# Kernel tuning notes

Hardware: AMD Instinct MI355X
Metric: run time of the kernel (lower is better)

Reference implementation:

```python
import jax, jax.numpy as jnp
import numpy as np

N = 16        # n_var
L = 16        # max_lags
H = 16        # hidden_dim
B = 32768     # batch
G = N * N     # n_var^2 groups


def setup_inputs() -> dict:
    key = jax.random.key(0)
    ks = jax.random.split(key, 8)
    x = jax.random.normal(ks[0], (B, G, L), dtype=jnp.float32)
    causal = jax.random.randint(ks[1], (N, N, L), 0, 2, dtype=jnp.int32)
    # torch Conv1d init: U(-sqrt(k), sqrt(k)), k = 1/(in_channels_per_group*kernel)
    s1 = 1.0 / np.sqrt(L)        # conv1: in/group=1, kernel=L
    s2 = 1.0 / np.sqrt(H)        # conv2: in/group=H, kernel=1
    s3 = 1.0 / np.sqrt(N * H)    # conv3: in/group=N*H, kernel=1
    W1 = jax.random.uniform(ks[2], (G, H, L), jnp.float32, -s1, s1)
    b1 = jax.random.uniform(ks[3], (G, H), jnp.float32, -s1, s1)
    W2 = jax.random.uniform(ks[4], (G, H, H), jnp.float32, -s2, s2)
    b2 = jax.random.uniform(ks[5], (G, H), jnp.float32, -s2, s2)
    W3 = jax.random.uniform(ks[6], (N, N * H), jnp.float32, -s3, s3)
    b3 = jax.random.uniform(ks[7], (N,), jnp.float32, -s3, s3)
    return {"x": x, "causal": causal, "W1": W1, "b1": b1,
            "W2": W2, "b2": b2, "W3": W3, "b3": b3}


def reference(x, causal, W1, b1, W2, b2, W3, b3):
    # mask = ~causal_matrix.bool() -> masked_fill with 0 == multiply by causal!=0
    mask = (causal != 0).reshape(1, G, L).astype(x.dtype)
    xm = x * mask                                          # [B, G, L]
    # conv1: per-group (1 -> H) over the full lag window (output length 1)
    h1 = jax.nn.sigmoid(jnp.einsum('bgl,ghl->bgh', xm, W1) + b1)   # [B, G, H]
    # conv2: per-group (H -> H) 1x1; W2[g, out, in]
    h2 = jax.nn.sigmoid(jnp.einsum('bgh,gkh->bgk', h1, W2) + b2)   # [B, G, H]
    # conv3: groups = n_var, per variable (N*H -> 1) 1x1
    h2f = h2.reshape(-1, N, N * H)                          # [B, N, N*H]
    out = jnp.einsum('bvm,vm->bv', h2f, W3) + b3            # [B, N]
    return out
```

## Files before the change

kernel.cpp:

```cpp
#include <hip/hip_runtime.h>
#include <hip/hip_bf16.h>

#define N_VAR 16
#define LAGS  16
#define HID   16
#define GRP   256
#define BATCH 32768

typedef __attribute__((ext_vector_type(8))) short  bf16x8;
typedef __attribute__((ext_vector_type(4))) short  short4v;
typedef __attribute__((ext_vector_type(4))) float  floatx4;

__device__ __forceinline__ float sigmoid_fast(float t) {
    float e = __expf(-t);
    return __builtin_amdgcn_rcpf(1.0f + e);
}

__device__ __forceinline__ short f2bf(float f) {
    __hip_bfloat16 h = __float2bfloat16(f);
    return __builtin_bit_cast(short, h);
}

__global__ __launch_bounds__(256) void prep_weights(
    const float* __restrict__ W1, const float* __restrict__ W2,
    const int* __restrict__ causal,
    short* __restrict__ W1b, short* __restrict__ W2b)
{
    const int i = blockIdx.x * 256 + threadIdx.x;
    const int g = i >> 8;
    const int l = i & 15;
    const float msk = (causal[g * LAGS + l] != 0) ? 1.0f : 0.0f;
    W1b[i] = f2bf(W1[i] * msk);
    W2b[i] = f2bf(W2[i]);
}

__global__ __launch_bounds__(256) void additive_mfma(
    const float* __restrict__ x,
    const float* __restrict__ b1,
    const float* __restrict__ b2,
    const float* __restrict__ W3,
    const float* __restrict__ b3,
    const short* __restrict__ W1b,
    const short* __restrict__ W2b,
    float* __restrict__ out)
{
    const int lane = threadIdx.x & 63;
    const int w    = blockIdx.x * 4 + (threadIdx.x >> 6);
    const int v    = w & (N_VAR - 1);
    const int b0   = (w >> 4) * 16;
    const int m    = lane & 15;
    const int q    = lane >> 4;

    const float* __restrict__ xbase = x + (size_t)(b0 + m) * (GRP * LAGS) + q * 4;
    const float  b3v = b3[v];
    float acc = 0.0f;

    for (int n = 0; n < N_VAR; ++n) {
        const int g = v * N_VAR + n;

        const floatx4 xv = *reinterpret_cast<const floatx4*>(xbase + g * LAGS);
        bf16x8 fx = {f2bf(xv[0]), f2bf(xv[1]), f2bf(xv[2]), f2bf(xv[3]),
                     (short)0, (short)0, (short)0, (short)0};

        const short4v w1v = *reinterpret_cast<const short4v*>(
            W1b + (g * HID + m) * LAGS + q * 4);
        bf16x8 fa1 = {w1v[0], w1v[1], w1v[2], w1v[3],
                      (short)0, (short)0, (short)0, (short)0};

        floatx4 c1 = *reinterpret_cast<const floatx4*>(b1 + g * HID + q * 4);

        floatx4 d1 = __builtin_amdgcn_mfma_f32_16x16x32_bf16(fa1, fx, c1, 0, 0, 0);

        bf16x8 fb2 = {f2bf(sigmoid_fast(d1[0])), f2bf(sigmoid_fast(d1[1])),
                      f2bf(sigmoid_fast(d1[2])), f2bf(sigmoid_fast(d1[3])),
                      (short)0, (short)0, (short)0, (short)0};

        const short4v w2v = *reinterpret_cast<const short4v*>(
            W2b + (g * HID + m) * HID + q * 4);
        bf16x8 fa2 = {w2v[0], w2v[1], w2v[2], w2v[3],
                      (short)0, (short)0, (short)0, (short)0};

        floatx4 c2 = *reinterpret_cast<const floatx4*>(b2 + g * HID + q * 4);

        floatx4 d2 = __builtin_amdgcn_mfma_f32_16x16x32_bf16(fa2, fb2, c2, 0, 0, 0);

        const floatx4 w3v = *reinterpret_cast<const floatx4*>(
            W3 + v * (N_VAR * HID) + n * HID + q * 4);
        acc += sigmoid_fast(d2[0]) * w3v[0];
        acc += sigmoid_fast(d2[1]) * w3v[1];
        acc += sigmoid_fast(d2[2]) * w3v[2];
        acc += sigmoid_fast(d2[3]) * w3v[3];
    }

    acc += __shfl_xor(acc, 16);
    acc += __shfl_xor(acc, 32);
    if (lane < 16)
        out[(size_t)(b0 + lane) * N_VAR + v] = acc + b3v;
}

extern "C" void kernel_launch(void* const* d_in, const int* in_sizes, int n_in,
                              void* d_out, int out_size, void* d_ws, size_t ws_size,
                              hipStream_t stream) {
    const float* x      = (const float*)d_in[0];
    const int*   causal = (const int*)  d_in[1];
    const float* W1     = (const float*)d_in[2];
    const float* b1     = (const float*)d_in[3];
    const float* W2     = (const float*)d_in[4];
    const float* b2     = (const float*)d_in[5];
    const float* W3     = (const float*)d_in[6];
    const float* b3     = (const float*)d_in[7];
    float* out          = (float*)d_out;

    short* W1b = (short*)d_ws;
    short* W2b = (short*)d_ws + GRP * HID * LAGS;

    prep_weights<<<(GRP * HID * LAGS) / 256, 256, 0, stream>>>(
        W1, W2, causal, W1b, W2b);

    const int n_waves  = (BATCH / 16) * N_VAR;
    const int n_blocks = n_waves / 4;
    additive_mfma<<<n_blocks, 256, 0, stream>>>(
        x, b1, b2, W3, b3, W1b, W2b, out);
}
```

Before: 726.4 us.

## Stage per-variable weights in LDS and prefetch x loads across iterations

Each block now handles a single variable v for 64 batch rows, so all four waves share the same weights. The block stages W1b, W2b, b1, b2 and W3 in padded shared memory once, where before every wave fetched them from global or L2 on each iteration. The x loop is software-pipelined to load the next two groups' x vectors while the current two are processed, which hides global latency. In exchange the kernel adds LDS usage, a block barrier and more registers, which may lower occupancy.

```diff
diff --git a/kernel.cpp b/kernel.cpp
--- a/kernel.cpp
+++ b/kernel.cpp
@@ -6,6 +6,7 @@
 #define HID   16
 #define GRP   256
 #define BATCH 32768
+#define WPAD  20
 
 typedef __attribute__((ext_vector_type(8))) short  bf16x8;
 typedef __attribute__((ext_vector_type(4))) short  short4v;
@@ -44,52 +45,88 @@
     const short* __restrict__ W2b,
     float* __restrict__ out)
 {
-    const int lane = threadIdx.x & 63;
-    const int w    = blockIdx.x * 4 + (threadIdx.x >> 6);
-    const int v    = w & (N_VAR - 1);
-    const int b0   = (w >> 4) * 16;
+    __shared__ short w1s[16][16][WPAD];
+    __shared__ short w2s[16][16][WPAD];
+    __shared__ float b1s[16][16];
+    __shared__ float b2s[16][16];
+    __shared__ float w3s[16][16];
+
+    const int t    = threadIdx.x;
+    const int v    = blockIdx.x & (N_VAR - 1);
+    const int bb   = blockIdx.x >> 4;
+    const int widx = t >> 6;
+    const int lane = t & 63;
     const int m    = lane & 15;
     const int q    = lane >> 4;
+    const int b0   = bb * 64 + widx * 16;
 
-    const float* __restrict__ xbase = x + (size_t)(b0 + m) * (GRP * LAGS) + q * 4;
-    const float  b3v = b3[v];
+    {
+        const int n  = t >> 4;
+        const int hh = t & 15;
+        const short* s1 = W1b + (((v * N_VAR + n) * HID) + hh) * LAGS;
+        const short* s2 = W2b + (((v * N_VAR + n) * HID) + hh) * HID;
+        #pragma unroll
+        for (int j = 0; j < 4; ++j) {
+            *reinterpret_cast<short4v*>(&w1s[n][hh][j * 4]) =
+                *reinterpret_cast<const short4v*>(s1 + j * 4);
+            *reinterpret_cast<short4v*>(&w2s[n][hh][j * 4]) =
+                *reinterpret_cast<const short4v*>(s2 + j * 4);
+        }
+        (&b1s[0][0])[t] = b1[v * GRP + t];
+        (&b2s[0][0])[t] = b2[v * GRP + t];
+        (&w3s[0][0])[t] = W3[v * (N_VAR * HID) + t];
+    }
+    __syncthreads();
+
+    const float* __restrict__ xp =
+        x + (size_t)(b0 + m) * (GRP * LAGS) + v * (N_VAR * LAGS) + q * 4;
+    const float b3v = b3[v];
     float acc = 0.0f;
 
-    for (int n = 0; n < N_VAR; ++n) {
-        const int g = v * N_VAR + n;
+    const short* w1p = &w1s[0][m][q * 4];
+    const short* w2p = &w2s[0][m][q * 4];
+    const float* b1p = &b1s[0][q * 4];
+    const float* b2p = &b2s[0][q * 4];
+    const float* w3p = &w3s[0][q * 4];
 
-        const floatx4 xv = *reinterpret_cast<const floatx4*>(xbase + g * LAGS);
-        bf16x8 fx = {f2bf(xv[0]), f2bf(xv[1]), f2bf(xv[2]), f2bf(xv[3]),
-                     (short)0, (short)0, (short)0, (short)0};
-
-        const short4v w1v = *reinterpret_cast<const short4v*>(
-            W1b + (g * HID + m) * LAGS + q * 4);
+    auto process = [&](int n, floatx4 xv) {
+        const short4v w1v = *reinterpret_cast<const short4v*>(w1p + n * (16 * WPAD));
         bf16x8 fa1 = {w1v[0], w1v[1], w1v[2], w1v[3],
                       (short)0, (short)0, (short)0, (short)0};
-
-        floatx4 c1 = *reinterpret_cast<const floatx4*>(b1 + g * HID + q * 4);
-
+        bf16x8 fx  = {f2bf(xv[0]), f2bf(xv[1]), f2bf(xv[2]), f2bf(xv[3]),
+                      (short)0, (short)0, (short)0, (short)0};
+        floatx4 c1 = *reinterpret_cast<const floatx4*>(b1p + n * 16);
         floatx4 d1 = __builtin_amdgcn_mfma_f32_16x16x32_bf16(fa1, fx, c1, 0, 0, 0);
 
         bf16x8 fb2 = {f2bf(sigmoid_fast(d1[0])), f2bf(sigmoid_fast(d1[1])),
                       f2bf(sigmoid_fast(d1[2])), f2bf(sigmoid_fast(d1[3])),
                       (short)0, (short)0, (short)0, (short)0};
-
-        const short4v w2v = *reinterpret_cast<const short4v*>(
-            W2b + (g * HID + m) * HID + q * 4);
+        const short4v w2v = *reinterpret_cast<const short4v*>(w2p + n * (16 * WPAD));
         bf16x8 fa2 = {w2v[0], w2v[1], w2v[2], w2v[3],
                       (short)0, (short)0, (short)0, (short)0};
-
-        floatx4 c2 = *reinterpret_cast<const floatx4*>(b2 + g * HID + q * 4);
-
+        floatx4 c2 = *reinterpret_cast<const floatx4*>(b2p + n * 16);
         floatx4 d2 = __builtin_amdgcn_mfma_f32_16x16x32_bf16(fa2, fb2, c2, 0, 0, 0);
 
-        const floatx4 w3v = *reinterpret_cast<const floatx4*>(
-            W3 + v * (N_VAR * HID) + n * HID + q * 4);
+        const floatx4 w3v = *reinterpret_cast<const floatx4*>(w3p + n * 16);
         acc += sigmoid_fast(d2[0]) * w3v[0];
         acc += sigmoid_fast(d2[1]) * w3v[1];
         acc += sigmoid_fast(d2[2]) * w3v[2];
         acc += sigmoid_fast(d2[3]) * w3v[3];
+    };
+
+    floatx4 cur0 = *reinterpret_cast<const floatx4*>(xp);
+    floatx4 cur1 = *reinterpret_cast<const floatx4*>(xp + LAGS);
+
+    #pragma unroll 1
+    for (int np = 0; np < 8; ++np) {
+        floatx4 nxt0, nxt1;
+        if (np < 7) {
+            nxt0 = *reinterpret_cast<const floatx4*>(xp + (2 * np + 2) * LAGS);
+            nxt1 = *reinterpret_cast<const floatx4*>(xp + (2 * np + 3) * LAGS);
+        }
+        process(2 * np,     cur0);
+        process(2 * np + 1, cur1);
+        if (np < 7) { cur0 = nxt0; cur1 = nxt1; }
     }
 
     acc += __shfl_xor(acc, 16);
@@ -117,8 +154,7 @@
     prep_weights<<<(GRP * HID * LAGS) / 256, 256, 0, stream>>>(
         W1, W2, causal, W1b, W2b);
 
-    const int n_waves  = (BATCH / 16) * N_VAR;
-    const int n_blocks = n_waves / 4;
+    const int n_blocks = (BATCH / 64) * N_VAR;
     additive_mfma<<<n_blocks, 256, 0, stream>>>(
         x, b1, b2, W3, b3, W1b, W2b, out);
 }
```

Result: faster. 693.7 us (-4.5%).
